# Kernel optimization log

Hardware: AMD Instinct MI355X
Metric: run time of the kernel (lower is better)

Reference implementation:

```python
import jax, jax.numpy as jnp
import numpy as np

HID = 2048
HEAD = 64
NH = HID // HEAD  # 32 heads
B, T = 4, 2048


def setup_inputs() -> dict:
    key = jax.random.key(0)
    ks = jax.random.split(key, 32)
    def n(i, shape, sc):
        return (jax.random.normal(ks[i], shape, jnp.float32) * sc).astype(jnp.float32)
    return {
        "hidden": n(0, (B, T, HID), 1.0),
        "attn_x": n(1, (B, HID), 1.0),
        "attn_kv": n(2, (B, NH, HEAD, HEAD), 0.1),
        "ffn_x": n(3, (B, HID), 1.0),
        "time_maa_x": n(4, (1, 1, HID), 0.5),
        "time_maa_w": n(5, (1, 1, HID), 0.5),
        "time_maa_k": n(6, (1, 1, HID), 0.5),
        "time_maa_v": n(7, (1, 1, HID), 0.5),
        "time_maa_r": n(8, (1, 1, HID), 0.5),
        "time_maa_g": n(9, (1, 1, HID), 0.5),
        "time_maa_w1": n(10, (HID, 160), 0.02),
        "time_maa_w2": n(11, (5, 32, HID), 0.02),
        "time_decay": n(12, (1, 1, HID), 0.5),
        "time_decay_w1": n(13, (HID, 64), 0.02),
        "time_decay_w2": n(14, (64, HID), 0.02),
        "time_faaaa": n(15, (NH, HEAD), 0.5),
        "receptance_w": n(16, (HID, HID), 0.02),
        "key_w": n(17, (HID, HID), 0.02),
        "value_w": n(18, (HID, HID), 0.02),
        "gate_w": n(19, (HID, HID), 0.02),
        "output_w": n(20, (HID, HID), 0.02),
        "gn_gamma": 1.0 + n(21, (HID,), 0.1),
        "gn_beta": n(22, (HID,), 0.1),
    }


def reference(hidden, attn_x, attn_kv, ffn_x,
              time_maa_x, time_maa_w, time_maa_k, time_maa_v, time_maa_r, time_maa_g,
              time_maa_w1, time_maa_w2, time_decay, time_decay_w1, time_decay_w2,
              time_faaaa, receptance_w, key_w, value_w, gate_w, output_w,
              gn_gamma, gn_beta):
    Bb, Tt, C = hidden.shape
    x = hidden
    shifted = jnp.concatenate([attn_x[:, None, :], x[:, :-1, :]], axis=1)
    dx = shifted - x
    time_mix = x + dx * time_maa_x
    # token-shift LoRA: (B,T,C)@(C,160) -> (5,B*T,32)@(5,32,C) -> five mixes
    xxx = jnp.tanh(time_mix @ time_maa_w1).reshape(Bb * Tt, 5, 32).transpose(1, 0, 2)
    xxx = jnp.einsum('nbk,nkc->nbc', xxx, time_maa_w2)
    mw, mk, mv, mr, mg = xxx.reshape(5, Bb, Tt, C)
    xw = x + dx * (time_maa_w + mw)
    xk = x + dx * (time_maa_k + mk)
    xv = x + dx * (time_maa_v + mv)
    xr = x + dx * (time_maa_r + mr)
    xg = x + dx * (time_maa_g + mg)
    r = (xr @ receptance_w).reshape(Bb, Tt, NH, HEAD).transpose(0, 2, 1, 3)  # (B,H,T,hs)
    k = (xk @ key_w).reshape(Bb, Tt, NH, HEAD).transpose(0, 2, 1, 3)
    v = (xv @ value_w).reshape(Bb, Tt, NH, HEAD).transpose(0, 2, 1, 3)
    g = jax.nn.silu(xg @ gate_w)
    td = time_decay + jnp.tanh(xw @ time_decay_w1) @ time_decay_w2  # (B,T,C)
    w = jnp.exp(-jnp.exp(td)).reshape(Bb, Tt, NH, HEAD).transpose(0, 2, 1, 3)
    # Source updates layer_state only AFTER the time loop, so inside the loop the
    # state is the constant attn_kv:  out_t = r_t @ (u * (k_t v_t^T) + S0).
    rk = jnp.einsum('bhtd,hd,bhtd->bht', r, time_faaaa, k)
    out = rk[..., None] * v + jnp.einsum('bhtd,bhde->bhte', r, attn_kv)  # (B,H,T,hs)
    new_attn_kv = k[:, :, -1, :, None] * v[:, :, -1, None, :] + w[:, :, -1, :, None] * attn_kv
    new_attn_x = hidden[:, -1]
    out = out.transpose(0, 2, 1, 3).reshape(Bb, Tt, C)
    # keras GroupNormalization(groups=NH) on (B,T,C): stats over (T, within-group channels)
    go = out.reshape(Bb, Tt, NH, HEAD)
    mean = go.mean(axis=(1, 3), keepdims=True)
    var = go.var(axis=(1, 3), keepdims=True)
    eps = 1e-5 * HEAD ** 2
    out = ((go - mean) * jax.lax.rsqrt(var + eps)).reshape(Bb, Tt, C) * gn_gamma + gn_beta
    out = (out * g) @ output_w
    return out, new_attn_x, new_attn_kv, ffn_x
```

## Files before the change

### kernel.cpp

```cpp
#include <hip/hip_runtime.h>

#define HID 2048
#define TSEQ 2048
#define BBATCH 4
#define MROWS 8192
#define NHEADS 32

typedef float fvec4 __attribute__((ext_vector_type(4)));
typedef unsigned short usvec4 __attribute__((ext_vector_type(4)));
typedef unsigned short usvec8 __attribute__((ext_vector_type(8)));
typedef __bf16 bh8 __attribute__((ext_vector_type(8)));
typedef float f32x4 __attribute__((ext_vector_type(4)));

__device__ __forceinline__ float bf2f(unsigned short u){
  return __uint_as_float(((unsigned int)u) << 16);
}
__device__ __forceinline__ unsigned short f2bf(float f){
  unsigned int u = __float_as_uint(f);
  return (unsigned short)((u + 0x7fffu + ((u >> 16) & 1u)) >> 16);
}
__device__ __forceinline__ void gll16(const void* g, void* lds){
  __builtin_amdgcn_global_load_lds(
      (const __attribute__((address_space(1))) unsigned int*)g,
      (__attribute__((address_space(3))) unsigned int*)lds, 16, 0, 0);
}

#define PIPE_SYNC(NSTR)                                              \
  asm volatile("s_waitcnt vmcnt(" NSTR ")\n\ts_barrier" ::: "memory"); \
  __builtin_amdgcn_sched_barrier(0);

__global__ void tcast_kernel(const float* __restrict__ in, unsigned short* __restrict__ out,
                             int R, int C){
  __shared__ float tile[32][33];
  int c0 = blockIdx.x * 32, r0 = blockIdx.y * 32;
  int tx = threadIdx.x, ty = threadIdx.y;
  for (int i = ty; i < 32; i += 8){
    int r = r0 + i, c = c0 + tx;
    tile[i][tx] = (r < R && c < C) ? in[(size_t)r * C + c] : 0.f;
  }
  __syncthreads();
  for (int i = ty; i < 32; i += 8){
    int c = c0 + i, r = r0 + tx;
    if (c < C && r < R) out[(size_t)c * R + r] = f2bf(tile[tx][i]);
  }
}

__global__ void zero_stats_kernel(float* __restrict__ gsum, float* __restrict__ gsqs){
  int i = threadIdx.x;
  gsum[i] = 0.f;
  gsqs[i] = 0.f;
}

__global__ void tmix_kernel(const float* __restrict__ hidden, const float* __restrict__ attn_x,
                            const float* __restrict__ tmx, unsigned short* __restrict__ tm){
  int i4 = blockIdx.x * 256 + threadIdx.x;
  int row = i4 >> 9;
  int c4 = i4 & 511;
  fvec4 x = *(const fvec4*)&hidden[(size_t)i4 * 4];
  fvec4 p;
  if ((row & (TSEQ - 1)) == 0){
    int b = row >> 11;
    p = *(const fvec4*)&attn_x[b * HID + c4 * 4];
  } else {
    p = *(const fvec4*)&hidden[(size_t)(i4 - 512) * 4];
  }
  fvec4 tx = *(const fvec4*)&tmx[c4 * 4];
  fvec4 t = x + (p - x) * tx;
  usvec4 o;
  o[0]=f2bf(t[0]); o[1]=f2bf(t[1]); o[2]=f2bf(t[2]); o[3]=f2bf(t[3]);
  *(usvec4*)&tm[(size_t)i4 * 4] = o;
}

template<int ACT, int OUTBF16>
__global__ __launch_bounds__(256, 2) void gemm_kernel(
    const unsigned short* __restrict__ A, const unsigned short* __restrict__ Bt,
    void* __restrict__ Cptr, int M, int N, int K, int ldc)
{
  __shared__ unsigned short As[128 * 32];
  __shared__ unsigned short Bs[128 * 32];
  const int tid = threadIdx.x;
  const int lane = tid & 63;
  const int w = tid >> 6;
  const int wr = w >> 1, wc = w & 1;
  const int lr = lane & 15, lq = lane >> 4;
  const int rowBase = blockIdx.y * 128;
  const int colBase = blockIdx.x * 128;

  const int arow = tid >> 2;
  const int ach = tid & 3;
  const unsigned short* aptr0 = A + (size_t)(rowBase + arow) * K + ach * 8;
  const unsigned short* aptr1 = aptr0 + (size_t)64 * K;
  int br0 = colBase + arow;      if (br0 > N - 1) br0 = N - 1;
  int br1 = colBase + arow + 64; if (br1 > N - 1) br1 = N - 1;
  const unsigned short* bptr0 = Bt + (size_t)br0 * K + ach * 8;
  const unsigned short* bptr1 = Bt + (size_t)br1 * K + ach * 8;

  f32x4 acc[4][4] = {};

  const int nk = K >> 5;
  for (int kk = 0; kk < nk; ++kk){
    gll16(aptr0, &As[tid * 8]);
    gll16(aptr1, &As[(tid + 256) * 8]);
    gll16(bptr0, &Bs[tid * 8]);
    gll16(bptr1, &Bs[(tid + 256) * 8]);
    aptr0 += 32; aptr1 += 32; bptr0 += 32; bptr1 += 32;
    __syncthreads();
    bh8 af[4], bfv[4];
    #pragma unroll
    for (int m = 0; m < 4; ++m)
      af[m] = *reinterpret_cast<const bh8*>(&As[(wr * 64 + m * 16 + lr) * 32 + lq * 8]);
    #pragma unroll
    for (int n = 0; n < 4; ++n)
      bfv[n] = *reinterpret_cast<const bh8*>(&Bs[(wc * 64 + n * 16 + lr) * 32 + lq * 8]);
    #pragma unroll
    for (int m = 0; m < 4; ++m)
      #pragma unroll
      for (int n = 0; n < 4; ++n)
        acc[m][n] = __builtin_amdgcn_mfma_f32_16x16x32_bf16(af[m], bfv[n], acc[m][n], 0, 0, 0);
    __syncthreads();
  }

  #pragma unroll
  for (int m = 0; m < 4; ++m){
    int gr0 = rowBase + wr * 64 + m * 16 + lq * 4;
    #pragma unroll
    for (int n = 0; n < 4; ++n){
      int gc = colBase + wc * 64 + n * 16 + lr;
      if (gc < N){
        #pragma unroll
        for (int q = 0; q < 4; ++q){
          float v = acc[m][n][q];
          if constexpr (ACT == 1) v = tanhf(v);
          else if constexpr (ACT == 2) v = v / (1.0f + __expf(-v));
          size_t off = (size_t)(gr0 + q) * ldc + gc;
          if constexpr (OUTBF16) ((unsigned short*)Cptr)[off] = f2bf(v);
          else                   ((float*)Cptr)[off] = v;
        }
      }
    }
  }
}

template<int ACT, int OUTBF16>
__global__ __launch_bounds__(512, 2) void gemm256_kernel(
    const unsigned short* __restrict__ A, const unsigned short* __restrict__ Bt,
    void* __restrict__ Cptr, int K)
{
  __shared__ unsigned short smem[65536];
  const int tid = threadIdx.x;
  const int lane = tid & 63, w = tid >> 6;
  const int wr = w >> 2, wc = w & 3;
  const int lr = lane & 15, lq = lane >> 4;

  const int bid = blockIdx.y * gridDim.x + blockIdx.x;
  const int xcd = bid & 7, qq = bid >> 3;
  const int by = xcd * 4 + (qq >> 3);
  const int bx = qq & 7;
  const int rowBase = by * 256;
  const int colBase = bx * 256;
  const int N = gridDim.x * 256;

  const unsigned short* srcA[2]; const unsigned short* srcB[2];
  int dstA[2], dstB[2];
  #pragma unroll
  for (int l = 0; l < 2; ++l){
    int ci = l * 512 + tid;
    int r = ci >> 2, c = ci & 3;
    int g = c ^ ((r >> 1) & 3);
    srcA[l] = A  + (size_t)(rowBase + r) * K + g * 8;
    srcB[l] = Bt + (size_t)(colBase + r) * K + g * 8;
    dstA[l] = ci * 8;
    dstB[l] = 8192 + ci * 8;
  }

  f32x4 acc[8][4] = {};
  const int ksel = (lq ^ ((lr >> 1) & 3)) * 8;

  auto STAGE = [&](int t, int bi){
    unsigned short* buf = smem + bi * 16384;
    #pragma unroll
    for (int l = 0; l < 2; ++l){
      gll16(srcA[l] + (size_t)t * 32, buf + dstA[l]);
      gll16(srcB[l] + (size_t)t * 32, buf + dstB[l]);
    }
  };

  auto COMPUTE = [&](int bi){
    const unsigned short* aB = smem + bi * 16384;
    const unsigned short* bB = aB + 8192;
    bh8 af[8], bf[4];
    #pragma unroll
    for (int m = 0; m < 8; ++m)
      af[m] = *reinterpret_cast<const bh8*>(&aB[(wr * 128 + m * 16 + lr) * 32 + ksel]);
    #pragma unroll
    for (int n = 0; n < 4; ++n)
      bf[n] = *reinterpret_cast<const bh8*>(&bB[(wc * 64 + n * 16 + lr) * 32 + ksel]);
    __builtin_amdgcn_s_setprio(1);
    #pragma unroll
    for (int m = 0; m < 8; ++m)
      #pragma unroll
      for (int n = 0; n < 4; ++n)
        acc[m][n] = __builtin_amdgcn_mfma_f32_16x16x32_bf16(af[m], bf[n], acc[m][n], 0, 0, 0);
    __builtin_amdgcn_s_setprio(0);
  };

  const int nt = K >> 5;
  STAGE(0, 0); STAGE(1, 1); STAGE(2, 2);
  PIPE_SYNC("8");
  for (int t = 0; t < nt - 3; ++t){
    STAGE(t + 3, (t + 3) & 3);
    COMPUTE(t & 3);
    PIPE_SYNC("8");
  }
  COMPUTE((nt - 3) & 3);
  PIPE_SYNC("4");
  COMPUTE((nt - 2) & 3);
  PIPE_SYNC("0");
  COMPUTE((nt - 1) & 3);

  #pragma unroll
  for (int m = 0; m < 8; ++m){
    int gr0 = rowBase + wr * 128 + m * 16 + lq * 4;
    #pragma unroll
    for (int n = 0; n < 4; ++n){
      int gc = colBase + wc * 64 + n * 16 + lr;
      #pragma unroll
      for (int q = 0; q < 4; ++q){
        float v = acc[m][n][q];
        if constexpr (ACT == 1) v = tanhf(v);
        else if constexpr (ACT == 2) v = v / (1.0f + __expf(-v));
        size_t off = (size_t)(gr0 + q) * N + gc;
        if constexpr (OUTBF16) ((unsigned short*)Cptr)[off] = f2bf(v);
        else                   ((float*)Cptr)[off] = v;
      }
    }
  }
}

__global__ __launch_bounds__(256) void mix_kernel(
    const float* __restrict__ xxx, const float* __restrict__ hidden,
    const float* __restrict__ attn_x, const float* __restrict__ w2,
    const float* __restrict__ tmk, const float* __restrict__ tmv,
    const float* __restrict__ tmr, const float* __restrict__ tmg,
    unsigned short* __restrict__ xk, unsigned short* __restrict__ xv,
    unsigned short* __restrict__ xr, unsigned short* __restrict__ xg)
{
  __shared__ __attribute__((aligned(16))) unsigned short smem[20992];
  unsigned short* xs   = smem;
  unsigned short* w2t  = smem + 10752;
  unsigned short* out4 = smem;

  const int tid = threadIdx.x;
  const int r0 = blockIdx.y * 64, c0 = blockIdx.x * 64;
  const int w = tid >> 6, lane = tid & 63, lr = lane & 15, lq = lane >> 4;

  for (int idx = tid; idx < 64 * 40; idx += 256){
    int r = idx / 40, cq = idx - r * 40;
    fvec4 v = *(const fvec4*)&xxx[(size_t)(r0 + r) * 160 + cq * 4];
    usvec4 o;
    o[0]=f2bf(v[0]); o[1]=f2bf(v[1]); o[2]=f2bf(v[2]); o[3]=f2bf(v[3]);
    *(usvec4*)&xs[r * 168 + cq * 4] = o;
  }
  for (int idx = tid; idx < 4 * 32 * 16; idx += 256){
    int n = idx >> 9;
    int rem = idx & 511;
    int j = rem >> 4, cq = rem & 15;
    fvec4 v = *(const fvec4*)&w2[(size_t)((n + 1) * 32 + j) * HID + c0 + cq * 4];
    #pragma unroll
    for (int cc = 0; cc < 4; ++cc)
      w2t[(n * 64 + cq * 4 + cc) * 40 + j] = f2bf(v[cc]);
  }
  __syncthreads();

  f32x4 acc[4][4] = {};
  #pragma unroll
  for (int n = 0; n < 4; ++n){
    bh8 afr = *reinterpret_cast<const bh8*>(&xs[(w * 16 + lr) * 168 + (n + 1) * 32 + lq * 8]);
    #pragma unroll
    for (int ct = 0; ct < 4; ++ct){
      bh8 bfr = *reinterpret_cast<const bh8*>(&w2t[(n * 64 + ct * 16 + lr) * 40 + lq * 8]);
      acc[ct][n] = __builtin_amdgcn_mfma_f32_16x16x32_bf16(afr, bfr, acc[ct][n], 0, 0, 0);
    }
  }
  __syncthreads();

  #pragma unroll
  for (int ct = 0; ct < 4; ++ct){
    int gc = c0 + ct * 16 + lr;
    float tk_ = tmk[gc], tv_ = tmv[gc], tr_ = tmr[gc], tg_ = tmg[gc];
    #pragma unroll
    for (int q = 0; q < 4; ++q){
      int row64 = w * 16 + lq * 4 + q;
      int gr = r0 + row64;
      size_t rowoff = (size_t)gr * HID + gc;
      float xx = hidden[rowoff];
      float pp = ((gr & (TSEQ - 1)) == 0) ? attn_x[(gr >> 11) * HID + gc]
                                          : hidden[rowoff - HID];
      float dxv = pp - xx;
      int lo = row64 * 72 + ct * 16 + lr;
      out4[(0 * 64 * 72) + lo] = f2bf(xx + dxv * (tk_ + acc[ct][0][q]));
      out4[(1 * 64 * 72) + lo] = f2bf(xx + dxv * (tv_ + acc[ct][1][q]));
      out4[(2 * 64 * 72) + lo] = f2bf(xx + dxv * (tr_ + acc[ct][2][q]));
      out4[(3 * 64 * 72) + lo] = f2bf(xx + dxv * (tg_ + acc[ct][3][q]));
    }
  }
  __syncthreads();

  #pragma unroll
  for (int a = 0; a < 4; ++a){
    unsigned short* dst = (a == 0) ? xk : (a == 1) ? xv : (a == 2) ? xr : xg;
    #pragma unroll
    for (int pass = 0; pass < 2; ++pass){
      int row64 = pass * 32 + (tid >> 3);
      int c8 = (tid & 7) * 8;
      usvec8 v8 = *(const usvec8*)&out4[(a * 64 + row64) * 72 + c8];
      *(usvec8*)&dst[(size_t)(r0 + row64) * HID + c0 + c8] = v8;
    }
  }
}

__global__ __launch_bounds__(256) void attn_kernel(
    const unsigned short* __restrict__ rb, const unsigned short* __restrict__ kb,
    const unsigned short* __restrict__ vb, const float* __restrict__ attn_kv,
    const float* __restrict__ faaaa, unsigned short* __restrict__ out0b,
    float* __restrict__ gsum, float* __restrict__ gsqs)
{
  const int bh = blockIdx.y;
  const int b = bh >> 5, h = bh & 31;
  const int tid = threadIdx.x, lane = tid & 63, w = tid >> 6;
  const int lr = lane & 15, lq = lane >> 4;
  const int t0 = blockIdx.x * 256 + w * 64;
  const size_t rowbase = (size_t)(b * TSEQ + t0) * HID + h * 64;

  const float* akvp = attn_kv + (size_t)bh * 4096;
  bh8 bfr[2][4];
  #pragma unroll
  for (int kk = 0; kk < 2; ++kk)
    #pragma unroll
    for (int n = 0; n < 4; ++n)
      #pragma unroll
      for (int j = 0; j < 8; ++j)
        bfr[kk][n][j] = (__bf16)akvp[(kk * 32 + lq * 8 + j) * 64 + n * 16 + lr];

  float fa0[8], fa1[8];
  #pragma unroll
  for (int j = 0; j < 8; ++j){
    fa0[j] = faaaa[h * 64 + lq * 8 + j];
    fa1[j] = faaaa[h * 64 + 32 + lq * 8 + j];
  }

  __shared__ __attribute__((aligned(16))) float rk_s[4][64];
  __shared__ __attribute__((aligned(16))) unsigned short outb[4][64][72];

  f32x4 acc[4][4] = {};
  #pragma unroll
  for (int m = 0; m < 4; ++m){
    size_t ra = rowbase + (size_t)(m * 16 + lr) * HID;
    bh8 a0 = *reinterpret_cast<const bh8*>(&rb[ra + lq * 8]);
    bh8 a1 = *reinterpret_cast<const bh8*>(&rb[ra + 32 + lq * 8]);
    usvec8 k0 = *reinterpret_cast<const usvec8*>(&kb[ra + lq * 8]);
    usvec8 k1 = *reinterpret_cast<const usvec8*>(&kb[ra + 32 + lq * 8]);
    float p = 0.f;
    #pragma unroll
    for (int j = 0; j < 8; ++j){
      p += (float)a0[j] * fa0[j] * bf2f(k0[j]);
      p += (float)a1[j] * fa1[j] * bf2f(k1[j]);
    }
    p += __shfl_xor(p, 16, 64);
    p += __shfl_xor(p, 32, 64);
    if (lq == 0) rk_s[w][m * 16 + lr] = p;
    #pragma unroll
    for (int n = 0; n < 4; ++n){
      acc[m][n] = __builtin_amdgcn_mfma_f32_16x16x32_bf16(a0, bfr[0][n], acc[m][n], 0, 0, 0);
      acc[m][n] = __builtin_amdgcn_mfma_f32_16x16x32_bf16(a1, bfr[1][n], acc[m][n], 0, 0, 0);
    }
  }
  __syncthreads();

  float ssum = 0.f, ssq = 0.f;
  #pragma unroll
  for (int m = 0; m < 4; ++m){
    fvec4 rk4 = *(const fvec4*)&rk_s[w][m * 16 + lq * 4];
    #pragma unroll
    for (int n = 0; n < 4; ++n){
      int col = n * 16 + lr;
      #pragma unroll
      for (int q = 0; q < 4; ++q){
        int row = m * 16 + lq * 4 + q;
        float vv = bf2f(vb[rowbase + (size_t)row * HID + col]);
        float o = acc[m][n][q] + rk4[q] * vv;
        ssum += o; ssq += o * o;
        outb[w][row][col] = f2bf(o);
      }
    }
  }
  __syncthreads();
  #pragma unroll
  for (int pass = 0; pass < 8; ++pass){
    int row = pass * 8 + (lane >> 3);
    int c8 = (lane & 7) * 8;
    usvec8 o8 = *(const usvec8*)&outb[w][row][c8];
    *(usvec8*)&out0b[rowbase + (size_t)row * HID + c8] = o8;
  }
  #pragma unroll
  for (int off2 = 32; off2 > 0; off2 >>= 1){
    ssum += __shfl_xor(ssum, off2, 64);
    ssq  += __shfl_xor(ssq,  off2, 64);
  }
  if (lane == 0){ atomicAdd(&gsum[bh], ssum); atomicAdd(&gsqs[bh], ssq); }
}

__global__ void gn_stats_kernel(const float* __restrict__ gsum, const float* __restrict__ gsqs,
                                float* __restrict__ meaninv){
  int g = threadIdx.x;
  const float n = (float)(TSEQ * 64);
  float mean = gsum[g] / n;
  float var = gsqs[g] / n - mean * mean;
  meaninv[2 * g]     = mean;
  meaninv[2 * g + 1] = rsqrtf(var + 1e-5f * 64.0f * 64.0f);
}

__global__ void ynorm_kernel(const unsigned short* __restrict__ out0b,
                             const unsigned short* __restrict__ gb,
                             const float* __restrict__ meaninv, const float* __restrict__ gamma,
                             const float* __restrict__ beta, unsigned short* __restrict__ yb){
  int i4 = blockIdx.x * 256 + threadIdx.x;
  int row = i4 >> 9, c4 = i4 & 511;
  int b = row >> 11;
  int c = c4 * 4;
  int g = b * 32 + (c >> 6);
  float mean = meaninv[2 * g], inv = meaninv[2 * g + 1];
  usvec4 o4 = *(const usvec4*)&out0b[(size_t)i4 * 4];
  usvec4 gv = *(const usvec4*)&gb[(size_t)i4 * 4];
  fvec4 ga = *(const fvec4*)&gamma[c];
  fvec4 be = *(const fvec4*)&beta[c];
  usvec4 y;
  #pragma unroll
  for (int cc = 0; cc < 4; ++cc){
    float val = ((bf2f(o4[cc]) - mean) * inv * ga[cc] + be[cc]) * bf2f(gv[cc]);
    y[cc] = f2bf(val);
  }
  *(usvec4*)&yb[(size_t)i4 * 4] = y;
}

__global__ void lastrow_mix_kernel(const float* __restrict__ xxx, const float* __restrict__ hidden,
    const float* __restrict__ w2, const float* __restrict__ tmw, const float* __restrict__ tmk,
    const float* __restrict__ tmv, float* __restrict__ xw_l, float* __restrict__ xk_l,
    float* __restrict__ xv_l){
  int b = blockIdx.y;
  int c = blockIdx.x * 256 + threadIdx.x;
  __shared__ float xsr[160];
  int i = b * TSEQ + (TSEQ - 1);
  if (threadIdx.x < 160) xsr[threadIdx.x] = xxx[(size_t)i * 160 + threadIdx.x];
  __syncthreads();
  float mw = 0.f, mk = 0.f, mv = 0.f;
  for (int j = 0; j < 32; ++j){
    mw += xsr[j]      * w2[(size_t)(j)      * HID + c];
    mk += xsr[32 + j] * w2[(size_t)(32 + j) * HID + c];
    mv += xsr[64 + j] * w2[(size_t)(64 + j) * HID + c];
  }
  float x = hidden[(size_t)i * HID + c];
  float prev = hidden[(size_t)(i - 1) * HID + c];
  float dx = prev - x;
  xw_l[b * HID + c] = x + dx * (tmw[c] + mw);
  xk_l[b * HID + c] = x + dx * (tmk[c] + mk);
  xv_l[b * HID + c] = x + dx * (tmv[c] + mv);
}

__global__ void decay1_part_kernel(const float* __restrict__ xw_l, const float* __restrict__ tdw1,
                                   float* __restrict__ dpart){
  int b = blockIdx.y;
  int chunk = blockIdx.x;
  int j = threadIdx.x & 63, sub = threadIdx.x >> 6;
  float s = 0.f;
  int cbase = chunk * 128 + sub * 32;
  for (int r = 0; r < 32; ++r){
    int c = cbase + r;
    s += xw_l[b * HID + c] * tdw1[(size_t)c * 64 + j];
  }
  __shared__ float red[4][64];
  red[sub][j] = s;
  __syncthreads();
  if (sub == 0)
    dpart[((size_t)b * 16 + chunk) * 64 + j] = red[0][j] + red[1][j] + red[2][j] + red[3][j];
}

__global__ void decay1_reduce_kernel(const float* __restrict__ dpart, float* __restrict__ hdec){
  int tid = threadIdx.x;
  int b = tid >> 6, j = tid & 63;
  float s = 0.f;
  #pragma unroll
  for (int chunk = 0; chunk < 16; ++chunk)
    s += dpart[((size_t)b * 16 + chunk) * 64 + j];
  hdec[b * 64 + j] = tanhf(s);
}

__global__ __launch_bounds__(256) void lastrow_kv_part_kernel(
    const float* __restrict__ xk_l, const float* __restrict__ xv_l,
    const float* __restrict__ keyw, const float* __restrict__ valw,
    float* __restrict__ kpart, float* __restrict__ vpart){
  int c = blockIdx.x * 256 + threadIdx.x;
  int chunk = blockIdx.y;
  __shared__ float xs[2][4][128];
  for (int i = threadIdx.x; i < 512; i += 256){
    int b = i >> 7, r = i & 127;
    xs[0][b][r] = xk_l[b * HID + chunk * 128 + r];
    xs[1][b][r] = xv_l[b * HID + chunk * 128 + r];
  }
  __syncthreads();
  float ka[4] = {0,0,0,0}, va[4] = {0,0,0,0};
  for (int r = 0; r < 128; ++r){
    int c2 = chunk * 128 + r;
    float kw = keyw[(size_t)c2 * HID + c];
    float vw = valw[(size_t)c2 * HID + c];
    #pragma unroll
    for (int b = 0; b < 4; ++b){
      ka[b] += xs[0][b][r] * kw;
      va[b] += xs[1][b][r] * vw;
    }
  }
  #pragma unroll
  for (int b = 0; b < 4; ++b){
    kpart[((size_t)chunk * 4 + b) * HID + c] = ka[b];
    vpart[((size_t)chunk * 4 + b) * HID + c] = va[b];
  }
}

__global__ void lastrow_kv_reduce_kernel(
    const float* __restrict__ kpart, const float* __restrict__ vpart,
    const float* __restrict__ hdec, const float* __restrict__ tdw2,
    const float* __restrict__ tdecay, float* __restrict__ klast,
    float* __restrict__ vlast, float* __restrict__ wlast){
  int c = blockIdx.x * 256 + threadIdx.x;
  float ka[4] = {0,0,0,0}, va[4] = {0,0,0,0};
  for (int chunk = 0; chunk < 16; ++chunk){
    #pragma unroll
    for (int b = 0; b < 4; ++b){
      ka[b] += kpart[((size_t)chunk * 4 + b) * HID + c];
      va[b] += vpart[((size_t)chunk * 4 + b) * HID + c];
    }
  }
  float tdc = tdecay[c];
  float td[4] = {tdc, tdc, tdc, tdc};
  for (int j = 0; j < 64; ++j){
    float w2v = tdw2[(size_t)j * HID + c];
    #pragma unroll
    for (int b = 0; b < 4; ++b) td[b] += hdec[b * 64 + j] * w2v;
  }
  #pragma unroll
  for (int b = 0; b < 4; ++b){
    klast[b * HID + c] = ka[b];
    vlast[b * HID + c] = va[b];
    wlast[b * HID + c] = expf(-expf(td[b]));
  }
}

__global__ void newkv_kernel(const float* __restrict__ klast, const float* __restrict__ vlast,
    const float* __restrict__ wlast, const float* __restrict__ attn_kv,
    float* __restrict__ outkv){
  int idx = blockIdx.x * 256 + threadIdx.x;
  int b = idx >> 17;
  int h = (idx >> 12) & 31;
  int d = (idx >> 6) & 63;
  int e = idx & 63;
  float kl = klast[b * HID + h * 64 + d];
  float vl = vlast[b * HID + h * 64 + e];
  float wl = wlast[b * HID + h * 64 + d];
  outkv[idx] = kl * vl + wl * attn_kv[idx];
}

__global__ void copies_kernel(const float* __restrict__ hidden, const float* __restrict__ ffnx,
                              float* __restrict__ out_attnx, float* __restrict__ out_ffnx){
  int i = blockIdx.x * 256 + threadIdx.x;
  if (i < BBATCH * HID){
    int b = i >> 11, c = i & 2047;
    out_attnx[i] = hidden[((size_t)(b * TSEQ + TSEQ - 1)) * HID + c];
    out_ffnx[i] = ffnx[i];
  }
}

extern "C" void kernel_launch(void* const* d_in, const int* in_sizes, int n_in,
                              void* d_out, int out_size, void* d_ws, size_t ws_size,
                              hipStream_t stream)
{
  (void)in_sizes; (void)n_in; (void)out_size;
  const float* hidden = (const float*)d_in[0];
  const float* attn_x = (const float*)d_in[1];
  const float* attn_kv = (const float*)d_in[2];
  const float* ffn_x = (const float*)d_in[3];
  const float* tmaa_x = (const float*)d_in[4];
  const float* tmaa_w = (const float*)d_in[5];
  const float* tmaa_k = (const float*)d_in[6];
  const float* tmaa_v = (const float*)d_in[7];
  const float* tmaa_r = (const float*)d_in[8];
  const float* tmaa_g = (const float*)d_in[9];
  const float* w1 = (const float*)d_in[10];
  const float* w2 = (const float*)d_in[11];
  const float* tdecay = (const float*)d_in[12];
  const float* tdw1 = (const float*)d_in[13];
  const float* tdw2 = (const float*)d_in[14];
  const float* faaaa = (const float*)d_in[15];
  const float* recw = (const float*)d_in[16];
  const float* keyw = (const float*)d_in[17];
  const float* valw = (const float*)d_in[18];
  const float* gatew = (const float*)d_in[19];
  const float* outw = (const float*)d_in[20];
  const float* gamma = (const float*)d_in[21];
  const float* beta = (const float*)d_in[22];

  float* out_main  = (float*)d_out;
  float* out_attnx = out_main + (size_t)16777216;
  float* out_kv    = out_attnx + 8192;
  float* out_ffn   = out_kv + 524288;

  unsigned short* wr_t = (unsigned short*)d_out;
  unsigned short* wk_t = wr_t + (size_t)4194304;
  unsigned short* wv_t = wk_t + (size_t)4194304;
  unsigned short* wg_t = wv_t + (size_t)4194304;
  unsigned short* out0b = (unsigned short*)d_out;

  char* ws = (char*)d_ws;
  size_t off = 0;
  auto alloc = [&](size_t bytes) -> void* {
    void* p = ws + off; off += (bytes + 255) & ~(size_t)255; return p;
  };
  unsigned short* wo_t = (unsigned short*)alloc(2048ull * 2048 * 2);
  unsigned short* w1_t = (unsigned short*)alloc(160ull * 2048 * 2);
  float* xxx           = (float*)alloc((size_t)MROWS * 160 * 4);
  unsigned short* bufA = (unsigned short*)alloc((size_t)MROWS * HID * 2);
  unsigned short* bufB = (unsigned short*)alloc((size_t)MROWS * HID * 2);
  unsigned short* bufC = (unsigned short*)alloc((size_t)MROWS * HID * 2);
  unsigned short* bufD = (unsigned short*)alloc((size_t)MROWS * HID * 2);
  unsigned short* bufE = (unsigned short*)alloc((size_t)MROWS * HID * 2);
  float* gsum    = (float*)alloc(128 * 4);
  float* gsqs    = (float*)alloc(128 * 4);
  float* meaninv = (float*)alloc(256 * 4);
  float* xw_l  = (float*)alloc(BBATCH * HID * 4);
  float* xk_l  = (float*)alloc(BBATCH * HID * 4);
  float* xv_l  = (float*)alloc(BBATCH * HID * 4);
  float* klast = (float*)alloc(BBATCH * HID * 4);
  float* vlast = (float*)alloc(BBATCH * HID * 4);
  float* wlast = (float*)alloc(BBATCH * HID * 4);
  float* hdec  = (float*)alloc(BBATCH * 64 * 4);
  float* kpart = (float*)alloc(16ull * BBATCH * HID * 4);
  float* vpart = (float*)alloc(16ull * BBATCH * HID * 4);
  float* dpart = (float*)alloc((size_t)BBATCH * 16 * 64 * 4);

  if (off > ws_size) return;

  unsigned short* tm = bufA;
  unsigned short* xg = bufA;
  unsigned short* xr = bufB;
  unsigned short* kb = bufB;
  unsigned short* yb = bufB;
  unsigned short* xk = bufC;
  unsigned short* vb = bufC;
  unsigned short* xv = bufD;
  unsigned short* gb = bufD;
  unsigned short* rb = bufE;

  dim3 tb(32, 8);
  tcast_kernel<<<dim3(64, 64), tb, 0, stream>>>(recw,  wr_t, 2048, 2048);
  tcast_kernel<<<dim3(64, 64), tb, 0, stream>>>(keyw,  wk_t, 2048, 2048);
  tcast_kernel<<<dim3(64, 64), tb, 0, stream>>>(valw,  wv_t, 2048, 2048);
  tcast_kernel<<<dim3(64, 64), tb, 0, stream>>>(gatew, wg_t, 2048, 2048);
  tcast_kernel<<<dim3(64, 64), tb, 0, stream>>>(outw,  wo_t, 2048, 2048);
  tcast_kernel<<<dim3(5, 64),  tb, 0, stream>>>(w1,    w1_t, 2048, 160);
  zero_stats_kernel<<<1, 128, 0, stream>>>(gsum, gsqs);

  tmix_kernel<<<16384, 256, 0, stream>>>(hidden, attn_x, tmaa_x, tm);

  gemm_kernel<1, 0><<<dim3(2, 64), 256, 0, stream>>>(tm, w1_t, xxx, MROWS, 160, HID, 160);

  mix_kernel<<<dim3(32, 128), 256, 0, stream>>>(xxx, hidden, attn_x, w2,
      tmaa_k, tmaa_v, tmaa_r, tmaa_g, xk, xv, xr, xg);

  gemm256_kernel<0, 1><<<dim3(8, 32), 512, 0, stream>>>(xr, wr_t, rb, HID);
  gemm256_kernel<0, 1><<<dim3(8, 32), 512, 0, stream>>>(xk, wk_t, kb, HID);
  gemm256_kernel<0, 1><<<dim3(8, 32), 512, 0, stream>>>(xv, wv_t, vb, HID);
  gemm256_kernel<2, 1><<<dim3(8, 32), 512, 0, stream>>>(xg, wg_t, gb, HID);

  attn_kernel<<<dim3(8, 128), 256, 0, stream>>>(rb, kb, vb, attn_kv, faaaa,
                                                out0b, gsum, gsqs);
  gn_stats_kernel<<<1, 128, 0, stream>>>(gsum, gsqs, meaninv);
  ynorm_kernel<<<16384, 256, 0, stream>>>(out0b, gb, meaninv, gamma, beta, yb);

  gemm256_kernel<0, 0><<<dim3(8, 32), 512, 0, stream>>>(yb, wo_t, out_main, HID);

  lastrow_mix_kernel<<<dim3(8, 4), 256, 0, stream>>>(xxx, hidden, w2, tmaa_w, tmaa_k, tmaa_v,
                                                     xw_l, xk_l, xv_l);
  decay1_part_kernel<<<dim3(16, 4), 256, 0, stream>>>(xw_l, tdw1, dpart);
  decay1_reduce_kernel<<<1, 256, 0, stream>>>(dpart, hdec);
  lastrow_kv_part_kernel<<<dim3(8, 16), 256, 0, stream>>>(xk_l, xv_l, keyw, valw, kpart, vpart);
  lastrow_kv_reduce_kernel<<<8, 256, 0, stream>>>(kpart, vpart, hdec, tdw2, tdecay,
                                                  klast, vlast, wlast);
  newkv_kernel<<<2048, 256, 0, stream>>>(klast, vlast, wlast, attn_kv, out_kv);
  copies_kernel<<<32, 256, 0, stream>>>(hidden, ffn_x, out_attnx, out_ffn);
}
```

Measured before the change: 695.9 us.

## Split GEMM K-tiles into A/B half-stages with interleaved loads and batch weight casts

The 256x256 bf16 GEMM main loop now stages A and B tiles as separate half-buffers in an 8-slot ring and issues loads five half-stages ahead. Each K-step is split into two MFMA phases, with a B-fragment reload and a new global-to-LDS load between them, so memory traffic overlaps compute more finely. The five 2048x2048 weight transpose-casts are merged into one launch with a z-dimension to cut launch overhead. The extra barriers per K-step add synchronisation cost, and the new vmcnt accounting has to match the deeper ring exactly.

```diff
diff --git a/kernel.cpp b/kernel.cpp
--- a/kernel.cpp
+++ b/kernel.cpp
@@ -24,10 +24,6 @@
       (const __attribute__((address_space(1))) unsigned int*)g,
       (__attribute__((address_space(3))) unsigned int*)lds, 16, 0, 0);
 }
-
-#define PIPE_SYNC(NSTR)                                              \
-  asm volatile("s_waitcnt vmcnt(" NSTR ")\n\ts_barrier" ::: "memory"); \
-  __builtin_amdgcn_sched_barrier(0);
 
 __global__ void tcast_kernel(const float* __restrict__ in, unsigned short* __restrict__ out,
                              int R, int C){
@@ -43,6 +39,30 @@
     int c = c0 + i, r = r0 + tx;
     if (c < C && r < R) out[(size_t)c * R + r] = f2bf(tile[tx][i]);
   }
+}
+
+__global__ void tcast5_kernel(const float* __restrict__ i0, const float* __restrict__ i1,
+                              const float* __restrict__ i2, const float* __restrict__ i3,
+                              const float* __restrict__ i4,
+                              unsigned short* __restrict__ o0, unsigned short* __restrict__ o1,
+                              unsigned short* __restrict__ o2, unsigned short* __restrict__ o3,
+                              unsigned short* __restrict__ o4){
+  const float* in; unsigned short* out;
+  switch (blockIdx.z){
+    case 0:  in = i0; out = o0; break;
+    case 1:  in = i1; out = o1; break;
+    case 2:  in = i2; out = o2; break;
+    case 3:  in = i3; out = o3; break;
+    default: in = i4; out = o4; break;
+  }
+  __shared__ float tile[32][33];
+  int c0 = blockIdx.x * 32, r0 = blockIdx.y * 32;
+  int tx = threadIdx.x, ty = threadIdx.y;
+  for (int i = ty; i < 32; i += 8)
+    tile[i][tx] = in[(size_t)(r0 + i) * 2048 + c0 + tx];
+  __syncthreads();
+  for (int i = ty; i < 32; i += 8)
+    out[(size_t)(c0 + i) * 2048 + r0 + tx] = f2bf(tile[tx][i]);
 }
 
 __global__ void zero_stats_kernel(float* __restrict__ gsum, float* __restrict__ gsqs){
@@ -160,63 +180,88 @@
   const int colBase = bx * 256;
   const int N = gridDim.x * 256;
 
-  const unsigned short* srcA[2]; const unsigned short* srcB[2];
-  int dstA[2], dstB[2];
-  #pragma unroll
-  for (int l = 0; l < 2; ++l){
-    int ci = l * 512 + tid;
+  const unsigned short* gA[2]; const unsigned short* gB[2];
+  int dstoff[2];
+  #pragma unroll
+  for (int ld = 0; ld < 2; ++ld){
+    int ci = ld * 512 + tid;
     int r = ci >> 2, c = ci & 3;
     int g = c ^ ((r >> 1) & 3);
-    srcA[l] = A  + (size_t)(rowBase + r) * K + g * 8;
-    srcB[l] = Bt + (size_t)(colBase + r) * K + g * 8;
-    dstA[l] = ci * 8;
-    dstB[l] = 8192 + ci * 8;
+    gA[ld] = A  + (size_t)(rowBase + r) * K + g * 8;
+    gB[ld] = Bt + (size_t)(colBase + r) * K + g * 8;
+    dstoff[ld] = ci * 8;
   }
 
   f32x4 acc[8][4] = {};
+  bh8 af[8], bfr[2];
   const int ksel = (lq ^ ((lr >> 1) & 3)) * 8;
 
-  auto STAGE = [&](int t, int bi){
-    unsigned short* buf = smem + bi * 16384;
-    #pragma unroll
-    for (int l = 0; l < 2; ++l){
-      gll16(srcA[l] + (size_t)t * 32, buf + dstA[l]);
-      gll16(srcB[l] + (size_t)t * 32, buf + dstB[l]);
+  auto STAGE = [&](int h){
+    int koff = (h >> 2) * 64 + ((h >> 1) & 1) * 32;
+    unsigned short* sb = smem + (h & 7) * 8192;
+    if (h & 1){
+      gll16(gB[0] + koff, sb + dstoff[0]);
+      gll16(gB[1] + koff, sb + dstoff[1]);
+    } else {
+      gll16(gA[0] + koff, sb + dstoff[0]);
+      gll16(gA[1] + koff, sb + dstoff[1]);
     }
   };
-
-  auto COMPUTE = [&](int bi){
-    const unsigned short* aB = smem + bi * 16384;
+  auto RDA = [&](const unsigned short* aB){
+    #pragma unroll
+    for (int m = 0; m < 8; ++m){
+      int row = wr * 128 + m * 16 + lr;
+      af[m] = *reinterpret_cast<const bh8*>(&aB[row * 32 + ksel]);
+    }
+  };
+  auto RDB = [&](const unsigned short* bB, int nh){
+    #pragma unroll
+    for (int i = 0; i < 2; ++i){
+      int row = wc * 64 + (nh * 2 + i) * 16 + lr;
+      bfr[i] = *reinterpret_cast<const bh8*>(&bB[row * 32 + ksel]);
+    }
+  };
+
+  const int nph = K >> 4;
+
+  STAGE(0); STAGE(1); STAGE(2); STAGE(3); STAGE(4);
+  asm volatile("s_waitcnt vmcnt(6)\n\ts_barrier" ::: "memory");
+  __builtin_amdgcn_sched_barrier(0);
+
+  for (int pp = 0; pp < (K >> 5); ++pp){
+    const int p0 = pp * 2;
+    const unsigned short* aB = smem + (size_t)(p0 & 6) * 8192;
     const unsigned short* bB = aB + 8192;
-    bh8 af[8], bf[4];
-    #pragma unroll
-    for (int m = 0; m < 8; ++m)
-      af[m] = *reinterpret_cast<const bh8*>(&aB[(wr * 128 + m * 16 + lr) * 32 + ksel]);
-    #pragma unroll
-    for (int n = 0; n < 4; ++n)
-      bf[n] = *reinterpret_cast<const bh8*>(&bB[(wc * 64 + n * 16 + lr) * 32 + ksel]);
+    { int h = p0 + 5; if (h < nph) STAGE(h); }
+    RDA(aB);
+    RDB(bB, 0);
+    asm volatile("s_barrier" ::: "memory");
+    asm volatile("s_waitcnt lgkmcnt(0)" ::: "memory");
+    __builtin_amdgcn_sched_barrier(0);
     __builtin_amdgcn_s_setprio(1);
     #pragma unroll
-    for (int m = 0; m < 8; ++m)
-      #pragma unroll
-      for (int n = 0; n < 4; ++n)
-        acc[m][n] = __builtin_amdgcn_mfma_f32_16x16x32_bf16(af[m], bf[n], acc[m][n], 0, 0, 0);
+    for (int m = 0; m < 8; ++m){
+      acc[m][0] = __builtin_amdgcn_mfma_f32_16x16x32_bf16(af[m], bfr[0], acc[m][0], 0, 0, 0);
+      acc[m][1] = __builtin_amdgcn_mfma_f32_16x16x32_bf16(af[m], bfr[1], acc[m][1], 0, 0, 0);
+    }
     __builtin_amdgcn_s_setprio(0);
-  };
-
-  const int nt = K >> 5;
-  STAGE(0, 0); STAGE(1, 1); STAGE(2, 2);
-  PIPE_SYNC("8");
-  for (int t = 0; t < nt - 3; ++t){
-    STAGE(t + 3, (t + 3) & 3);
-    COMPUTE(t & 3);
-    PIPE_SYNC("8");
-  }
-  COMPUTE((nt - 3) & 3);
-  PIPE_SYNC("4");
-  COMPUTE((nt - 2) & 3);
-  PIPE_SYNC("0");
-  COMPUTE((nt - 1) & 3);
+    asm volatile("s_barrier" ::: "memory");
+    __builtin_amdgcn_sched_barrier(0);
+    { int h = p0 + 6; if (h < nph) STAGE(h); }
+    RDB(bB, 1);
+    asm volatile("s_barrier" ::: "memory");
+    asm volatile("s_waitcnt lgkmcnt(0)" ::: "memory");
+    __builtin_amdgcn_sched_barrier(0);
+    __builtin_amdgcn_s_setprio(1);
+    #pragma unroll
+    for (int m = 0; m < 8; ++m){
+      acc[m][2] = __builtin_amdgcn_mfma_f32_16x16x32_bf16(af[m], bfr[0], acc[m][2], 0, 0, 0);
+      acc[m][3] = __builtin_amdgcn_mfma_f32_16x16x32_bf16(af[m], bfr[1], acc[m][3], 0, 0, 0);
+    }
+    __builtin_amdgcn_s_setprio(0);
+    asm volatile("s_waitcnt vmcnt(6)\n\ts_barrier" ::: "memory");
+    __builtin_amdgcn_sched_barrier(0);
+  }
 
   #pragma unroll
   for (int m = 0; m < 8; ++m){
@@ -660,11 +705,8 @@
   unsigned short* rb = bufE;
 
   dim3 tb(32, 8);
-  tcast_kernel<<<dim3(64, 64), tb, 0, stream>>>(recw,  wr_t, 2048, 2048);
-  tcast_kernel<<<dim3(64, 64), tb, 0, stream>>>(keyw,  wk_t, 2048, 2048);
-  tcast_kernel<<<dim3(64, 64), tb, 0, stream>>>(valw,  wv_t, 2048, 2048);
-  tcast_kernel<<<dim3(64, 64), tb, 0, stream>>>(gatew, wg_t, 2048, 2048);
-  tcast_kernel<<<dim3(64, 64), tb, 0, stream>>>(outw,  wo_t, 2048, 2048);
+  tcast5_kernel<<<dim3(64, 64, 5), tb, 0, stream>>>(recw, keyw, valw, gatew, outw,
+                                                    wr_t, wk_t, wv_t, wg_t, wo_t);
   tcast_kernel<<<dim3(5, 64),  tb, 0, stream>>>(w1,    w1_t, 2048, 160);
   zero_stats_kernel<<<1, 128, 0, stream>>>(gsum, gsqs);
 
```

After: 690.3 us. No clear change (-0.8%).
